# Kernel tuning notes

Measured on AMD Instinct MI355X. Metric: run time of the kernel, lower is better.

The kernel has to match this reference:

```python
import jax, jax.numpy as jnp
import numpy as np

N = 50000
E = 1600000
DIM = 128
RC = 5.0
DEPTH = 3


def setup_inputs() -> dict:
    key = jax.random.key(0)
    kv, ke, ks, kd, kw, kb, krs, ksig = jax.random.split(key, 8)
    v = jax.random.normal(kv, (N, DIM), dtype=jnp.float32)
    # edge distances in [0, rc]
    e = jax.random.uniform(ke, (E, 1), dtype=jnp.float32) * RC
    src = jax.random.randint(ks, (E,), 0, N, dtype=jnp.int32)
    dst = jax.random.randint(kd, (E,), 0, N, dtype=jnp.int32)
    # learned params: A = nn.Linear(dim, dim); rs, sigma = torch.rand(1)
    A_w = jax.random.normal(kw, (DIM, DIM), dtype=jnp.float32) / np.sqrt(DIM)
    A_b = jax.random.normal(kb, (DIM,), dtype=jnp.float32) * 0.01
    rs = jax.random.uniform(krs, (1,), dtype=jnp.float32)
    sigma = jax.random.uniform(ksig, (1,), dtype=jnp.float32)
    return {"v": v, "e": e, "src": src, "dst": dst,
            "A_w": A_w, "A_b": A_b, "rs": rs, "sigma": sigma}


def _edge_envelope(r, rs, sigma):
    # exp(-(r-rs)^2/sigma^2) * 0.5 * cos(pi*r/rc) * (r < rc)
    gauss = jnp.exp(-jnp.square(r - rs) / jnp.square(sigma))
    cutoff = 0.5 * jnp.cos(np.pi * r / RC) * (r < RC).astype(r.dtype)
    return gauss * cutoff


def reference(v, e, src, dst, A_w, A_b, rs, sigma):
    f = _edge_envelope(e, rs, sigma)  # [E, 1]
    cur = v
    for _ in range(DEPTH):
        msg = f * cur[src]  # gather src node feats, weight by edge envelope: [E, DIM]
        svf = jax.ops.segment_sum(msg, dst, num_segments=N)  # scatter-sum to dst: [N, DIM]
        cur = jax.nn.relu((svf + v) @ A_w.T + A_b)  # linear + relu, skip from original v
    return cur
```

## Files before the change

### kernel.cpp

```cpp
#include <hip/hip_runtime.h>
#include <math.h>

#define N_NODES 50000
#define N_PAD   50048
#define N_EDGES 1600000
#define DIM     128
#define RCUT    5.0f
#define NGROUP  (N_PAD / 64)
#define NB_PRE  512
#define CH_PRE  (N_EDGES / NB_PRE)
#define NB_CONV 6250
#define NB_WPREP 8

typedef __attribute__((ext_vector_type(8))) __bf16 bf16x8;
typedef __attribute__((ext_vector_type(4))) float  f32x4;

__device__ __forceinline__ float bf_lo(unsigned int u) { return __uint_as_float(u << 16); }
__device__ __forceinline__ float bf_hi(unsigned int u) { return __uint_as_float(u & 0xffff0000u); }
__device__ __forceinline__ unsigned short f2bf(float x) {
    unsigned int u = __float_as_uint(x);
    u += 0x7fffu + ((u >> 16) & 1u);
    return (unsigned short)(u >> 16);
}

__global__ __launch_bounds__(256) void preA_kernel(
        const float* __restrict__ v, unsigned short* __restrict__ vb,
        const float* __restrict__ Aw, uint4* __restrict__ wfrag,
        const int* __restrict__ dst, int* __restrict__ partial) {
    int b = blockIdx.x;
    if (b < NB_CONV) {
        int i = b * 256 + threadIdx.x;
        float4 x = ((const float4*)v)[i];
        uint2 o;
        o.x = (unsigned)f2bf(x.x) | ((unsigned)f2bf(x.y) << 16);
        o.y = (unsigned)f2bf(x.z) | ((unsigned)f2bf(x.w) << 16);
        ((uint2*)vb)[i] = o;
    } else if (b < NB_CONV + NB_WPREP) {
        int t = (b - NB_CONV) * 256 + threadIdx.x;
        int lane = t & 63, nt = (t >> 6) & 7, kk = t >> 9;
        int n  = nt * 16 + (lane & 15);
        int k0 = kk * 32 + (lane >> 4) * 8;
        unsigned short h[8];
        #pragma unroll
        for (int i = 0; i < 8; ++i) h[i] = f2bf(Aw[n * DIM + k0 + i]);
        uint4 o;
        o.x = h[0] | ((unsigned)h[1] << 16); o.y = h[2] | ((unsigned)h[3] << 16);
        o.z = h[4] | ((unsigned)h[5] << 16); o.w = h[6] | ((unsigned)h[7] << 16);
        wfrag[t] = o;
    } else {
        __shared__ int h[NGROUP];
        int cb = b - NB_CONV - NB_WPREP, tid = threadIdx.x;
        for (int g = tid; g < NGROUP; g += 256) h[g] = 0;
        __syncthreads();
        int beg = cb * CH_PRE, end = beg + CH_PRE;
        for (int i = beg + tid; i < end; i += 256)
            atomicAdd(&h[dst[i] >> 6], 1);
        __syncthreads();
        for (int g = tid; g < NGROUP; g += 256) partial[cb * NGROUP + g] = h[g];
    }
}

__global__ __launch_bounds__(256) void ktot_kernel(const int* __restrict__ partial,
                                                   int* __restrict__ gtot) {
    int g = blockIdx.x * 256 + threadIdx.x;
    if (g >= NGROUP) return;
    int s = 0;
    for (int b = 0; b < NB_PRE; ++b) s += partial[b * NGROUP + g];
    gtot[g] = s;
}

__global__ __launch_bounds__(256) void kscan_kernel(const int* __restrict__ gtot,
                                                    int* __restrict__ goff) {
    __shared__ int part[256];
    int tid = threadIdx.x;
    int i0 = tid * 4;
    int v[4]; int s = 0;
    #pragma unroll
    for (int k = 0; k < 4; ++k) { int i = i0 + k; v[k] = (i < NGROUP) ? gtot[i] : 0; s += v[k]; }
    part[tid] = s; __syncthreads();
    for (int d = 1; d < 256; d <<= 1) {
        int val = (tid >= d) ? part[tid - d] : 0;
        __syncthreads(); part[tid] += val; __syncthreads();
    }
    int run = (tid == 0) ? 0 : part[tid - 1];
    #pragma unroll
    for (int k = 0; k < 4; ++k) {
        int i = i0 + k;
        if (i < NGROUP) { goff[i] = run; run += v[k]; }
    }
    if (tid == 0) goff[NGROUP] = N_EDGES;
}

__global__ __launch_bounds__(256) void kbase_kernel(const int* __restrict__ partial,
                                                    const int* __restrict__ goff,
                                                    int* __restrict__ pbase) {
    int g = blockIdx.x * 256 + threadIdx.x;
    if (g >= NGROUP) return;
    int run = goff[g];
    for (int b = 0; b < NB_PRE; ++b) {
        pbase[b * NGROUP + g] = run;
        run += partial[b * NGROUP + g];
    }
}

__global__ __launch_bounds__(512) void reorder_kernel(
        const float* __restrict__ e,
        const int*   __restrict__ src,
        const int*   __restrict__ dst,
        const float* __restrict__ rs,
        const float* __restrict__ sigma,
        const int*   __restrict__ pbase,
        int2* __restrict__ metaT) {
    __shared__ int base[NGROUP];
    __shared__ int cnt[NGROUP];
    int b = blockIdx.x, tid = threadIdx.x;
    for (int g = tid; g < NGROUP; g += 512) { base[g] = pbase[b * NGROUP + g]; cnt[g] = 0; }
    __syncthreads();
    float rsv = rs[0], sg = sigma[0];
    int beg = b * CH_PRE, end = beg + CH_PRE;
    for (int i = beg + tid; i < end; i += 512) {
        float r  = e[i];
        float d  = r - rsv;
        float gauss = expf(-(d * d) / (sg * sg));
        float cut   = 0.5f * cosf(r * (float)(M_PI / (double)RCUT));
        cut = (r < RCUT) ? cut : 0.0f;
        float fe = gauss * cut;
        int dn = dst[i];
        int g  = dn >> 6;
        int lr = atomicAdd(&cnt[g], 1);
        metaT[base[g] + lr] = make_int2(src[i] * (DIM * 2) | ((dn & 63) << 24),
                                        __float_as_int(fe));
    }
}

__global__ __launch_bounds__(256) void tagsort_kernel(
        const int2* __restrict__ metaT,
        const int*  __restrict__ goff,
        int2* __restrict__ meta,
        int*  __restrict__ off) {
    __shared__ int cnt[64], base[64], cur[64];
    int g = blockIdx.x, tid = threadIdx.x;
    int sbeg = goff[g], send = goff[g + 1];
    if (tid < 64) cnt[tid] = 0;
    __syncthreads();
    for (int i = sbeg + tid; i < send; i += 256)
        atomicAdd(&cnt[(metaT[i].x >> 24) & 63], 1);
    __syncthreads();
    if (tid == 0) {
        int run = 0;
        #pragma unroll
        for (int t = 0; t < 64; ++t) { base[t] = run; cur[t] = run; run += cnt[t]; }
    }
    __syncthreads();
    if (tid < 64) {
        int node = g * 64 + tid;
        if (node <= N_NODES) off[node] = sbeg + base[tid];
    }
    __syncthreads();
    for (int i = sbeg + tid; i < send; i += 256) {
        int2 m = metaT[i];
        int tag = (m.x >> 24) & 63;
        int lr = atomicAdd(&cur[tag], 1);
        meta[sbeg + lr] = make_int2(m.x & 0x00FFFFFF, m.y);
    }
}

#define EDGE2(mx, mf, rr)                                        \
    do {                                                         \
        float ff = __int_as_float(mf);                           \
        a0 = fmaf(ff, bf_lo(rr), a0);                            \
        a1 = fmaf(ff, bf_hi(rr), a1);                            \
    } while (0)

__global__ __launch_bounds__(256) void gather_kernel(
        const unsigned short* __restrict__ cur,
        const unsigned short* __restrict__ vb,
        const int2*  __restrict__ meta,
        const int*   __restrict__ off,
        unsigned short* __restrict__ svf) {
    int n    = (blockIdx.x << 2) + (threadIdx.x >> 6);
    int lane = threadIdx.x & 63;

    unsigned vv = *(const unsigned*)((const char*)vb + (size_t)n * (DIM * 2) + lane * 4);
    float a0 = bf_lo(vv), a1 = bf_hi(vv);

    int beg = __builtin_amdgcn_readfirstlane(off[n]);
    int end = __builtin_amdgcn_readfirstlane(off[n + 1]);
    const char* base = (const char*)cur + lane * 4;

    int c = beg;
    if ((c & 1) && c < end) {
        int2 m = meta[c];
        unsigned rr = *(const unsigned*)(base + (unsigned)m.x);
        EDGE2(m.x, m.y, rr);
        ++c;
    }
    for (; c + 16 <= end; c += 16) {
        int4 m0 = *(const int4*)(meta + c);
        int4 m1 = *(const int4*)(meta + c + 2);
        int4 m2 = *(const int4*)(meta + c + 4);
        int4 m3 = *(const int4*)(meta + c + 6);
        int4 m4 = *(const int4*)(meta + c + 8);
        int4 m5 = *(const int4*)(meta + c + 10);
        int4 m6 = *(const int4*)(meta + c + 12);
        int4 m7 = *(const int4*)(meta + c + 14);
        unsigned r0  = *(const unsigned*)(base + (unsigned)m0.x);
        unsigned r1  = *(const unsigned*)(base + (unsigned)m0.z);
        unsigned r2  = *(const unsigned*)(base + (unsigned)m1.x);
        unsigned r3  = *(const unsigned*)(base + (unsigned)m1.z);
        unsigned r4  = *(const unsigned*)(base + (unsigned)m2.x);
        unsigned r5  = *(const unsigned*)(base + (unsigned)m2.z);
        unsigned r6  = *(const unsigned*)(base + (unsigned)m3.x);
        unsigned r7  = *(const unsigned*)(base + (unsigned)m3.z);
        unsigned r8  = *(const unsigned*)(base + (unsigned)m4.x);
        unsigned r9  = *(const unsigned*)(base + (unsigned)m4.z);
        unsigned r10 = *(const unsigned*)(base + (unsigned)m5.x);
        unsigned r11 = *(const unsigned*)(base + (unsigned)m5.z);
        unsigned r12 = *(const unsigned*)(base + (unsigned)m6.x);
        unsigned r13 = *(const unsigned*)(base + (unsigned)m6.z);
        unsigned r14 = *(const unsigned*)(base + (unsigned)m7.x);
        unsigned r15 = *(const unsigned*)(base + (unsigned)m7.z);
        EDGE2(m0.x, m0.y, r0);  EDGE2(m0.z, m0.w, r1);
        EDGE2(m1.x, m1.y, r2);  EDGE2(m1.z, m1.w, r3);
        EDGE2(m2.x, m2.y, r4);  EDGE2(m2.z, m2.w, r5);
        EDGE2(m3.x, m3.y, r6);  EDGE2(m3.z, m3.w, r7);
        EDGE2(m4.x, m4.y, r8);  EDGE2(m4.z, m4.w, r9);
        EDGE2(m5.x, m5.y, r10); EDGE2(m5.z, m5.w, r11);
        EDGE2(m6.x, m6.y, r12); EDGE2(m6.z, m6.w, r13);
        EDGE2(m7.x, m7.y, r14); EDGE2(m7.z, m7.w, r15);
    }
    if (c + 8 <= end) {
        int4 m0 = *(const int4*)(meta + c);
        int4 m1 = *(const int4*)(meta + c + 2);
        int4 m2 = *(const int4*)(meta + c + 4);
        int4 m3 = *(const int4*)(meta + c + 6);
        unsigned r0 = *(const unsigned*)(base + (unsigned)m0.x);
        unsigned r1 = *(const unsigned*)(base + (unsigned)m0.z);
        unsigned r2 = *(const unsigned*)(base + (unsigned)m1.x);
        unsigned r3 = *(const unsigned*)(base + (unsigned)m1.z);
        unsigned r4 = *(const unsigned*)(base + (unsigned)m2.x);
        unsigned r5 = *(const unsigned*)(base + (unsigned)m2.z);
        unsigned r6 = *(const unsigned*)(base + (unsigned)m3.x);
        unsigned r7 = *(const unsigned*)(base + (unsigned)m3.z);
        EDGE2(m0.x, m0.y, r0); EDGE2(m0.z, m0.w, r1);
        EDGE2(m1.x, m1.y, r2); EDGE2(m1.z, m1.w, r3);
        EDGE2(m2.x, m2.y, r4); EDGE2(m2.z, m2.w, r5);
        EDGE2(m3.x, m3.y, r6); EDGE2(m3.z, m3.w, r7);
        c += 8;
    }
    for (; c < end; ++c) {
        int2 m = meta[c];
        unsigned rr = *(const unsigned*)(base + (unsigned)m.x);
        EDGE2(m.x, m.y, rr);
    }
    unsigned o = (unsigned)f2bf(a0) | ((unsigned)f2bf(a1) << 16);
    *(unsigned*)(svf + (size_t)n * DIM + lane * 2) = o;
}

__global__ __launch_bounds__(256) void gemm_kernel(
        const unsigned short* __restrict__ X,
        const uint4* __restrict__ wfrag,
        const float* __restrict__ bias,
        unsigned short* __restrict__ out_bf,
        float* __restrict__ out_f,
        int last) {
    __shared__ uint4 wlds[2048];
    int tid = threadIdx.x;
    for (int i = tid; i < 2048; i += 256) wlds[i] = wfrag[i];

    int wv = tid >> 6, lane = tid & 63;
    int quad = lane >> 4, l16 = lane & 15;
    int row = blockIdx.x * 64 + wv * 16 + l16;

    f32x4 acc[8];
    #pragma unroll
    for (int i = 0; i < 8; ++i) acc[i] = (f32x4){0.f, 0.f, 0.f, 0.f};

    __syncthreads();

    const unsigned short* xp = X + (size_t)row * DIM + quad * 8;
    #pragma unroll
    for (int kk = 0; kk < 4; ++kk) {
        bf16x8 af = *(const bf16x8*)(xp + kk * 32);
        #pragma unroll
        for (int nt = 0; nt < 8; ++nt) {
            uint4 w = wlds[(kk * 8 + nt) * 64 + lane];
            bf16x8 bfr = __builtin_bit_cast(bf16x8, w);
            acc[nt] = __builtin_amdgcn_mfma_f32_16x16x32_bf16(af, bfr, acc[nt], 0, 0, 0);
        }
    }

    int orow0 = blockIdx.x * 64 + wv * 16 + quad * 4;
    #pragma unroll
    for (int nt = 0; nt < 8; ++nt) {
        int col = nt * 16 + l16;
        float b = bias[col];
        #pragma unroll
        for (int r = 0; r < 4; ++r) {
            int orow = orow0 + r;
            if (orow < N_NODES) {
                float val = fmaxf(acc[nt][r] + b, 0.f);
                if (last) out_f[(size_t)orow * DIM + col] = val;
                else      out_bf[(size_t)orow * DIM + col] = f2bf(val);
            }
        }
    }
}

extern "C" void kernel_launch(void* const* d_in, const int* in_sizes, int n_in,
                              void* d_out, int out_size, void* d_ws, size_t ws_size,
                              hipStream_t stream) {
    const float* v     = (const float*)d_in[0];
    const float* e     = (const float*)d_in[1];
    const int*   src   = (const int*)  d_in[2];
    const int*   dst   = (const int*)  d_in[3];
    const float* Aw    = (const float*)d_in[4];
    const float* Ab    = (const float*)d_in[5];
    const float* rs    = (const float*)d_in[6];
    const float* sigma = (const float*)d_in[7];
    float* out = (float*)d_out;

    char* p = (char*)d_ws;
    int2*           meta  = (int2*)p;            p += (size_t)N_EDGES * 8;
    unsigned short* bufV  = (unsigned short*)p;  p += (size_t)N_PAD * DIM * 2;
    unsigned short* bufA  = (unsigned short*)p;  p += (size_t)N_PAD * DIM * 2;
    unsigned short* bufB  = (unsigned short*)p;  p += (size_t)N_PAD * DIM * 2;
    uint4*          wfrag = (uint4*)p;           p += 2048 * 16;
    int*            off   = (int*)p;             p += (size_t)(N_NODES + 1) * 4;
    int*            gtot  = (int*)p;             p += (NGROUP + 2) * 4;
    int*            goff  = (int*)p;             p += (NGROUP + 2) * 4;
    int2* metaT   = (int2*)bufA;
    int*  partial = (int*)bufB;
    int*  pbase   = partial + NB_PRE * NGROUP;

    preA_kernel<<<NB_CONV + NB_WPREP + NB_PRE, 256, 0, stream>>>(
        v, bufV, Aw, wfrag, dst, partial);
    ktot_kernel<<<(NGROUP + 255) / 256, 256, 0, stream>>>(partial, gtot);
    kscan_kernel<<<1, 256, 0, stream>>>(gtot, goff);
    kbase_kernel<<<(NGROUP + 255) / 256, 256, 0, stream>>>(partial, goff, pbase);
    reorder_kernel<<<NB_PRE, 512, 0, stream>>>(e, src, dst, rs, sigma, pbase, metaT);
    tagsort_kernel<<<NGROUP, 256, 0, stream>>>(metaT, goff, meta, off);

    const int GB = N_NODES / 4;
    const int MB = N_PAD / 64;

    gather_kernel<<<GB, 256, 0, stream>>>(bufV, bufV, meta, off, bufA);
    gemm_kernel<<<MB, 256, 0, stream>>>(bufA, wfrag, Ab, bufB, nullptr, 0);
    gather_kernel<<<GB, 256, 0, stream>>>(bufB, bufV, meta, off, bufA);
    gemm_kernel<<<MB, 256, 0, stream>>>(bufA, wfrag, Ab, bufB, nullptr, 0);
    gather_kernel<<<GB, 256, 0, stream>>>(bufB, bufV, meta, off, bufA);
    gemm_kernel<<<MB, 256, 0, stream>>>(bufA, wfrag, Ab, nullptr, out, 1);
}
```

Baseline: 362.6 us.

## Fuse gather and GEMM into one layer kernel; parallelize prefix-count reductions

Each layer's gather-scatter-sum and the dense linear+ReLU are merged into one kernel. A 512-thread block aggregates 64 nodes into LDS as bf16 and then runs MFMA on them directly, so the bf16 intermediate no longer round-trips through global memory and three launches are dropped. The serial per-group reductions over 512 partial counts are split into 8 sub-blocks with a two-level sum to add parallelism in the CSR build. In exchange, weights are read from global or cache instead of LDS, and each wave processes 8 nodes serially, so gather parallelism per block falls and load balance changes. Buffers now ping-pong between bufB and bufA.

```diff
diff --git a/kernel.cpp b/kernel.cpp
--- a/kernel.cpp
+++ b/kernel.cpp
@@ -11,6 +11,9 @@
 #define CH_PRE  (N_EDGES / NB_PRE)
 #define NB_CONV 6250
 #define NB_WPREP 8
+#define NB_SUB  8
+#define B_SUB   (NB_PRE / NB_SUB)
+#define XPAD    136
 
 typedef __attribute__((ext_vector_type(8))) __bf16 bf16x8;
 typedef __attribute__((ext_vector_type(4))) float  f32x4;
@@ -60,23 +63,32 @@
     }
 }
 
-__global__ __launch_bounds__(256) void ktot_kernel(const int* __restrict__ partial,
-                                                   int* __restrict__ gtot) {
-    int g = blockIdx.x * 256 + threadIdx.x;
+__global__ __launch_bounds__(256) void ktot2_kernel(const int* __restrict__ partial,
+                                                    int* __restrict__ partial2) {
+    int gb = blockIdx.x & 3, bb = blockIdx.x >> 2;
+    int g = gb * 256 + threadIdx.x;
     if (g >= NGROUP) return;
     int s = 0;
-    for (int b = 0; b < NB_PRE; ++b) s += partial[b * NGROUP + g];
-    gtot[g] = s;
-}
-
-__global__ __launch_bounds__(256) void kscan_kernel(const int* __restrict__ gtot,
+    int b0 = bb * B_SUB;
+    for (int b = b0; b < b0 + B_SUB; ++b) s += partial[b * NGROUP + g];
+    partial2[bb * NGROUP + g] = s;
+}
+
+__global__ __launch_bounds__(256) void kscan_kernel(const int* __restrict__ partial2,
                                                     int* __restrict__ goff) {
     __shared__ int part[256];
     int tid = threadIdx.x;
     int i0 = tid * 4;
     int v[4]; int s = 0;
     #pragma unroll
-    for (int k = 0; k < 4; ++k) { int i = i0 + k; v[k] = (i < NGROUP) ? gtot[i] : 0; s += v[k]; }
+    for (int k = 0; k < 4; ++k) {
+        int i = i0 + k; int t = 0;
+        if (i < NGROUP) {
+            #pragma unroll
+            for (int bb = 0; bb < NB_SUB; ++bb) t += partial2[bb * NGROUP + i];
+        }
+        v[k] = t; s += t;
+    }
     part[tid] = s; __syncthreads();
     for (int d = 1; d < 256; d <<= 1) {
         int val = (tid >= d) ? part[tid - d] : 0;
@@ -91,13 +103,17 @@
     if (tid == 0) goff[NGROUP] = N_EDGES;
 }
 
-__global__ __launch_bounds__(256) void kbase_kernel(const int* __restrict__ partial,
-                                                    const int* __restrict__ goff,
-                                                    int* __restrict__ pbase) {
-    int g = blockIdx.x * 256 + threadIdx.x;
+__global__ __launch_bounds__(256) void kbase2_kernel(const int* __restrict__ partial,
+                                                     const int* __restrict__ partial2,
+                                                     const int* __restrict__ goff,
+                                                     int* __restrict__ pbase) {
+    int gb = blockIdx.x & 3, bb = blockIdx.x >> 2;
+    int g = gb * 256 + threadIdx.x;
     if (g >= NGROUP) return;
     int run = goff[g];
-    for (int b = 0; b < NB_PRE; ++b) {
+    for (int b2 = 0; b2 < bb; ++b2) run += partial2[b2 * NGROUP + g];
+    int b0 = bb * B_SUB;
+    for (int b = b0; b < b0 + B_SUB; ++b) {
         pbase[b * NGROUP + g] = run;
         run += partial[b * NGROUP + g];
     }
@@ -172,134 +188,137 @@
         a1 = fmaf(ff, bf_hi(rr), a1);                            \
     } while (0)
 
-__global__ __launch_bounds__(256) void gather_kernel(
+__global__ __launch_bounds__(512, 6) void layer_kernel(
         const unsigned short* __restrict__ cur,
         const unsigned short* __restrict__ vb,
         const int2*  __restrict__ meta,
         const int*   __restrict__ off,
-        unsigned short* __restrict__ svf) {
-    int n    = (blockIdx.x << 2) + (threadIdx.x >> 6);
-    int lane = threadIdx.x & 63;
-
-    unsigned vv = *(const unsigned*)((const char*)vb + (size_t)n * (DIM * 2) + lane * 4);
-    float a0 = bf_lo(vv), a1 = bf_hi(vv);
-
-    int beg = __builtin_amdgcn_readfirstlane(off[n]);
-    int end = __builtin_amdgcn_readfirstlane(off[n + 1]);
-    const char* base = (const char*)cur + lane * 4;
-
-    int c = beg;
-    if ((c & 1) && c < end) {
-        int2 m = meta[c];
-        unsigned rr = *(const unsigned*)(base + (unsigned)m.x);
-        EDGE2(m.x, m.y, rr);
-        ++c;
-    }
-    for (; c + 16 <= end; c += 16) {
-        int4 m0 = *(const int4*)(meta + c);
-        int4 m1 = *(const int4*)(meta + c + 2);
-        int4 m2 = *(const int4*)(meta + c + 4);
-        int4 m3 = *(const int4*)(meta + c + 6);
-        int4 m4 = *(const int4*)(meta + c + 8);
-        int4 m5 = *(const int4*)(meta + c + 10);
-        int4 m6 = *(const int4*)(meta + c + 12);
-        int4 m7 = *(const int4*)(meta + c + 14);
-        unsigned r0  = *(const unsigned*)(base + (unsigned)m0.x);
-        unsigned r1  = *(const unsigned*)(base + (unsigned)m0.z);
-        unsigned r2  = *(const unsigned*)(base + (unsigned)m1.x);
-        unsigned r3  = *(const unsigned*)(base + (unsigned)m1.z);
-        unsigned r4  = *(const unsigned*)(base + (unsigned)m2.x);
-        unsigned r5  = *(const unsigned*)(base + (unsigned)m2.z);
-        unsigned r6  = *(const unsigned*)(base + (unsigned)m3.x);
-        unsigned r7  = *(const unsigned*)(base + (unsigned)m3.z);
-        unsigned r8  = *(const unsigned*)(base + (unsigned)m4.x);
-        unsigned r9  = *(const unsigned*)(base + (unsigned)m4.z);
-        unsigned r10 = *(const unsigned*)(base + (unsigned)m5.x);
-        unsigned r11 = *(const unsigned*)(base + (unsigned)m5.z);
-        unsigned r12 = *(const unsigned*)(base + (unsigned)m6.x);
-        unsigned r13 = *(const unsigned*)(base + (unsigned)m6.z);
-        unsigned r14 = *(const unsigned*)(base + (unsigned)m7.x);
-        unsigned r15 = *(const unsigned*)(base + (unsigned)m7.z);
-        EDGE2(m0.x, m0.y, r0);  EDGE2(m0.z, m0.w, r1);
-        EDGE2(m1.x, m1.y, r2);  EDGE2(m1.z, m1.w, r3);
-        EDGE2(m2.x, m2.y, r4);  EDGE2(m2.z, m2.w, r5);
-        EDGE2(m3.x, m3.y, r6);  EDGE2(m3.z, m3.w, r7);
-        EDGE2(m4.x, m4.y, r8);  EDGE2(m4.z, m4.w, r9);
-        EDGE2(m5.x, m5.y, r10); EDGE2(m5.z, m5.w, r11);
-        EDGE2(m6.x, m6.y, r12); EDGE2(m6.z, m6.w, r13);
-        EDGE2(m7.x, m7.y, r14); EDGE2(m7.z, m7.w, r15);
-    }
-    if (c + 8 <= end) {
-        int4 m0 = *(const int4*)(meta + c);
-        int4 m1 = *(const int4*)(meta + c + 2);
-        int4 m2 = *(const int4*)(meta + c + 4);
-        int4 m3 = *(const int4*)(meta + c + 6);
-        unsigned r0 = *(const unsigned*)(base + (unsigned)m0.x);
-        unsigned r1 = *(const unsigned*)(base + (unsigned)m0.z);
-        unsigned r2 = *(const unsigned*)(base + (unsigned)m1.x);
-        unsigned r3 = *(const unsigned*)(base + (unsigned)m1.z);
-        unsigned r4 = *(const unsigned*)(base + (unsigned)m2.x);
-        unsigned r5 = *(const unsigned*)(base + (unsigned)m2.z);
-        unsigned r6 = *(const unsigned*)(base + (unsigned)m3.x);
-        unsigned r7 = *(const unsigned*)(base + (unsigned)m3.z);
-        EDGE2(m0.x, m0.y, r0); EDGE2(m0.z, m0.w, r1);
-        EDGE2(m1.x, m1.y, r2); EDGE2(m1.z, m1.w, r3);
-        EDGE2(m2.x, m2.y, r4); EDGE2(m2.z, m2.w, r5);
-        EDGE2(m3.x, m3.y, r6); EDGE2(m3.z, m3.w, r7);
-        c += 8;
-    }
-    for (; c < end; ++c) {
-        int2 m = meta[c];
-        unsigned rr = *(const unsigned*)(base + (unsigned)m.x);
-        EDGE2(m.x, m.y, rr);
-    }
-    unsigned o = (unsigned)f2bf(a0) | ((unsigned)f2bf(a1) << 16);
-    *(unsigned*)(svf + (size_t)n * DIM + lane * 2) = o;
-}
-
-__global__ __launch_bounds__(256) void gemm_kernel(
-        const unsigned short* __restrict__ X,
         const uint4* __restrict__ wfrag,
         const float* __restrict__ bias,
         unsigned short* __restrict__ out_bf,
         float* __restrict__ out_f,
         int last) {
-    __shared__ uint4 wlds[2048];
-    int tid = threadIdx.x;
-    for (int i = tid; i < 2048; i += 256) wlds[i] = wfrag[i];
-
-    int wv = tid >> 6, lane = tid & 63;
+    __shared__ unsigned short xlds[64 * XPAD];
+    int tid  = threadIdx.x;
+    int wv   = tid >> 6, lane = tid & 63;
+    int g    = blockIdx.x;
+    int n0   = g * 64 + wv * 8;
+
+    int offidx = n0 + ((lane < 9) ? lane : 8);
+    if (offidx > N_NODES) offidx = N_NODES;
+    int myoff = off[offidx];
+
+    const char* basec = (const char*)cur + lane * 4;
+
+    #pragma unroll 1
+    for (int q = 0; q < 8; ++q) {
+        int nl = wv * 8 + q;
+        int n  = n0 + q;
+        float a0 = 0.f, a1 = 0.f;
+        if (n < N_NODES) {
+            unsigned vv = *(const unsigned*)((const char*)vb + (size_t)n * (DIM * 2) + lane * 4);
+            a0 = bf_lo(vv); a1 = bf_hi(vv);
+            int beg = __builtin_amdgcn_readlane(myoff, q);
+            int end = __builtin_amdgcn_readlane(myoff, q + 1);
+            int c = beg;
+            if ((c & 1) && c < end) {
+                int2 m = meta[c];
+                unsigned rr = *(const unsigned*)(basec + (unsigned)m.x);
+                EDGE2(m.x, m.y, rr);
+                ++c;
+            }
+            for (; c + 16 <= end; c += 16) {
+                int4 m0 = *(const int4*)(meta + c);
+                int4 m1 = *(const int4*)(meta + c + 2);
+                int4 m2 = *(const int4*)(meta + c + 4);
+                int4 m3 = *(const int4*)(meta + c + 6);
+                int4 m4 = *(const int4*)(meta + c + 8);
+                int4 m5 = *(const int4*)(meta + c + 10);
+                int4 m6 = *(const int4*)(meta + c + 12);
+                int4 m7 = *(const int4*)(meta + c + 14);
+                unsigned r0  = *(const unsigned*)(basec + (unsigned)m0.x);
+                unsigned r1  = *(const unsigned*)(basec + (unsigned)m0.z);
+                unsigned r2  = *(const unsigned*)(basec + (unsigned)m1.x);
+                unsigned r3  = *(const unsigned*)(basec + (unsigned)m1.z);
+                unsigned r4  = *(const unsigned*)(basec + (unsigned)m2.x);
+                unsigned r5  = *(const unsigned*)(basec + (unsigned)m2.z);
+                unsigned r6  = *(const unsigned*)(basec + (unsigned)m3.x);
+                unsigned r7  = *(const unsigned*)(basec + (unsigned)m3.z);
+                unsigned r8  = *(const unsigned*)(basec + (unsigned)m4.x);
+                unsigned r9  = *(const unsigned*)(basec + (unsigned)m4.z);
+                unsigned r10 = *(const unsigned*)(basec + (unsigned)m5.x);
+                unsigned r11 = *(const unsigned*)(basec + (unsigned)m5.z);
+                unsigned r12 = *(const unsigned*)(basec + (unsigned)m6.x);
+                unsigned r13 = *(const unsigned*)(basec + (unsigned)m6.z);
+                unsigned r14 = *(const unsigned*)(basec + (unsigned)m7.x);
+                unsigned r15 = *(const unsigned*)(basec + (unsigned)m7.z);
+                EDGE2(m0.x, m0.y, r0);  EDGE2(m0.z, m0.w, r1);
+                EDGE2(m1.x, m1.y, r2);  EDGE2(m1.z, m1.w, r3);
+                EDGE2(m2.x, m2.y, r4);  EDGE2(m2.z, m2.w, r5);
+                EDGE2(m3.x, m3.y, r6);  EDGE2(m3.z, m3.w, r7);
+                EDGE2(m4.x, m4.y, r8);  EDGE2(m4.z, m4.w, r9);
+                EDGE2(m5.x, m5.y, r10); EDGE2(m5.z, m5.w, r11);
+                EDGE2(m6.x, m6.y, r12); EDGE2(m6.z, m6.w, r13);
+                EDGE2(m7.x, m7.y, r14); EDGE2(m7.z, m7.w, r15);
+            }
+            if (c + 8 <= end) {
+                int4 m0 = *(const int4*)(meta + c);
+                int4 m1 = *(const int4*)(meta + c + 2);
+                int4 m2 = *(const int4*)(meta + c + 4);
+                int4 m3 = *(const int4*)(meta + c + 6);
+                unsigned r0 = *(const unsigned*)(basec + (unsigned)m0.x);
+                unsigned r1 = *(const unsigned*)(basec + (unsigned)m0.z);
+                unsigned r2 = *(const unsigned*)(basec + (unsigned)m1.x);
+                unsigned r3 = *(const unsigned*)(basec + (unsigned)m1.z);
+                unsigned r4 = *(const unsigned*)(basec + (unsigned)m2.x);
+                unsigned r5 = *(const unsigned*)(basec + (unsigned)m2.z);
+                unsigned r6 = *(const unsigned*)(basec + (unsigned)m3.x);
+                unsigned r7 = *(const unsigned*)(basec + (unsigned)m3.z);
+                EDGE2(m0.x, m0.y, r0); EDGE2(m0.z, m0.w, r1);
+                EDGE2(m1.x, m1.y, r2); EDGE2(m1.z, m1.w, r3);
+                EDGE2(m2.x, m2.y, r4); EDGE2(m2.z, m2.w, r5);
+                EDGE2(m3.x, m3.y, r6); EDGE2(m3.z, m3.w, r7);
+                c += 8;
+            }
+            for (; c < end; ++c) {
+                int2 m = meta[c];
+                unsigned rr = *(const unsigned*)(basec + (unsigned)m.x);
+                EDGE2(m.x, m.y, rr);
+            }
+        }
+        *(unsigned*)(xlds + nl * XPAD + lane * 2) =
+            (unsigned)f2bf(a0) | ((unsigned)f2bf(a1) << 16);
+    }
+    __syncthreads();
+
     int quad = lane >> 4, l16 = lane & 15;
-    int row = blockIdx.x * 64 + wv * 16 + l16;
-
-    f32x4 acc[8];
-    #pragma unroll
-    for (int i = 0; i < 8; ++i) acc[i] = (f32x4){0.f, 0.f, 0.f, 0.f};
-
-    __syncthreads();
-
-    const unsigned short* xp = X + (size_t)row * DIM + quad * 8;
+    int rb = wv >> 1, nh = wv & 1;
+    f32x4 acc[4];
+    #pragma unroll
+    for (int j = 0; j < 4; ++j) acc[j] = (f32x4){0.f, 0.f, 0.f, 0.f};
+
+    const unsigned short* xp = xlds + (rb * 16 + l16) * XPAD + quad * 8;
     #pragma unroll
     for (int kk = 0; kk < 4; ++kk) {
         bf16x8 af = *(const bf16x8*)(xp + kk * 32);
         #pragma unroll
-        for (int nt = 0; nt < 8; ++nt) {
-            uint4 w = wlds[(kk * 8 + nt) * 64 + lane];
+        for (int j = 0; j < 4; ++j) {
+            uint4 w = wfrag[(kk * 8 + nh * 4 + j) * 64 + lane];
             bf16x8 bfr = __builtin_bit_cast(bf16x8, w);
-            acc[nt] = __builtin_amdgcn_mfma_f32_16x16x32_bf16(af, bfr, acc[nt], 0, 0, 0);
+            acc[j] = __builtin_amdgcn_mfma_f32_16x16x32_bf16(af, bfr, acc[j], 0, 0, 0);
         }
     }
 
-    int orow0 = blockIdx.x * 64 + wv * 16 + quad * 4;
-    #pragma unroll
-    for (int nt = 0; nt < 8; ++nt) {
-        int col = nt * 16 + l16;
+    int orow0 = g * 64 + rb * 16 + quad * 4;
+    #pragma unroll
+    for (int j = 0; j < 4; ++j) {
+        int col = (nh * 4 + j) * 16 + l16;
         float b = bias[col];
         #pragma unroll
         for (int r = 0; r < 4; ++r) {
             int orow = orow0 + r;
             if (orow < N_NODES) {
-                float val = fmaxf(acc[nt][r] + b, 0.f);
+                float val = fmaxf(acc[j][r] + b, 0.f);
                 if (last) out_f[(size_t)orow * DIM + col] = val;
                 else      out_bf[(size_t)orow * DIM + col] = f2bf(val);
             }
@@ -327,27 +346,21 @@
     unsigned short* bufB  = (unsigned short*)p;  p += (size_t)N_PAD * DIM * 2;
     uint4*          wfrag = (uint4*)p;           p += 2048 * 16;
     int*            off   = (int*)p;             p += (size_t)(N_NODES + 1) * 4;
-    int*            gtot  = (int*)p;             p += (NGROUP + 2) * 4;
     int*            goff  = (int*)p;             p += (NGROUP + 2) * 4;
-    int2* metaT   = (int2*)bufA;
-    int*  partial = (int*)bufB;
-    int*  pbase   = partial + NB_PRE * NGROUP;
+    int2* metaT    = (int2*)bufA;
+    int*  partial  = (int*)bufB;
+    int*  pbase    = partial + NB_PRE * NGROUP;
+    int*  partial2 = pbase + NB_PRE * NGROUP;
 
     preA_kernel<<<NB_CONV + NB_WPREP + NB_PRE, 256, 0, stream>>>(
         v, bufV, Aw, wfrag, dst, partial);
-    ktot_kernel<<<(NGROUP + 255) / 256, 256, 0, stream>>>(partial, gtot);
-    kscan_kernel<<<1, 256, 0, stream>>>(gtot, goff);
-    kbase_kernel<<<(NGROUP + 255) / 256, 256, 0, stream>>>(partial, goff, pbase);
+    ktot2_kernel<<<4 * NB_SUB, 256, 0, stream>>>(partial, partial2);
+    kscan_kernel<<<1, 256, 0, stream>>>(partial2, goff);
+    kbase2_kernel<<<4 * NB_SUB, 256, 0, stream>>>(partial, partial2, goff, pbase);
     reorder_kernel<<<NB_PRE, 512, 0, stream>>>(e, src, dst, rs, sigma, pbase, metaT);
     tagsort_kernel<<<NGROUP, 256, 0, stream>>>(metaT, goff, meta, off);
 
-    const int GB = N_NODES / 4;
-    const int MB = N_PAD / 64;
-
-    gather_kernel<<<GB, 256, 0, stream>>>(bufV, bufV, meta, off, bufA);
-    gemm_kernel<<<MB, 256, 0, stream>>>(bufA, wfrag, Ab, bufB, nullptr, 0);
-    gather_kernel<<<GB, 256, 0, stream>>>(bufB, bufV, meta, off, bufA);
-    gemm_kernel<<<MB, 256, 0, stream>>>(bufA, wfrag, Ab, bufB, nullptr, 0);
-    gather_kernel<<<GB, 256, 0, stream>>>(bufB, bufV, meta, off, bufA);
-    gemm_kernel<<<MB, 256, 0, stream>>>(bufA, wfrag, Ab, nullptr, out, 1);
-}
+    layer_kernel<<<NGROUP, 512, 0, stream>>>(bufV, bufV, meta, off, wfrag, Ab, bufB, nullptr, 0);
+    layer_kernel<<<NGROUP, 512, 0, stream>>>(bufB, bufV, meta, off, wfrag, Ab, bufA, nullptr, 0);
+    layer_kernel<<<NGROUP, 512, 0, stream>>>(bufA, bufV, meta, off, wfrag, Ab, nullptr, out, 1);
+}
```

After: 345.3 us. 4.8% less time.
